# Kernel optimization log

Measured on AMD Instinct MI355X. Metric: run time of the kernel, lower is better.

The kernel has to match this reference:

```python
import jax, jax.numpy as jnp
import numpy as np

HEADS, DIM_HEAD = 8, 64  # per init_kwargs


def cdist(x, w):
    """Euclidean distance between rows of x [..., n, d] and w [m, d] -> [..., n, m].
    Matches torch.cdist (non-squared) / L2DistanceLinear(squared=False)."""
    sq = (x * x).sum(-1, keepdims=True) + (w * w).sum(-1) - 2.0 * (x @ w.T)
    return jnp.sqrt(jnp.maximum(sq, 0.0))


def setup_inputs() -> dict:
    key = jax.random.key(0)
    k1, k2, k3 = jax.random.split(key, 3)
    B, N, D = 4, 2048, 512
    dim_inner = HEADS * DIM_HEAD  # 512
    x = jax.random.normal(k1, (B, N, D), dtype=jnp.float32)
    w_qkv = jax.random.normal(k2, (3 * dim_inner, D), dtype=jnp.float32)
    w_out = jax.random.normal(k3, (D, dim_inner), dtype=jnp.float32)
    return {"x": x, "w_qkv": w_qkv, "w_out": w_out}


def reference(x, w_qkv, w_out):
    B, N, D = x.shape
    scale = DIM_HEAD ** -0.5

    # L2-distance QKV projection (cdist, non-squared, no negate/bias)
    qkv = cdist(x, w_qkv)                                  # [B, N, 3*H*DH]
    qkv = qkv.reshape(B, N, 3, HEADS, DIM_HEAD).transpose(2, 0, 3, 1, 4)  # [3, B, H, N, DH]
    q, k, v = qkv[0], qkv[1], qkv[2]

    # neg squared-L2 attention scores: -(||q||^2 + ||k||^2 - 2 q.k)
    q_sq = (q * q).sum(-1)                                 # [B, H, N]
    k_sq = (k * k).sum(-1)                                 # [B, H, N]
    dots = jnp.einsum('bhid,bhjd->bhij', q, k)             # [B, H, N, N]
    sim = -(q_sq[..., :, None] + k_sq[..., None, :] - 2.0 * dots) * scale

    attn = jax.nn.softmax(sim, axis=-1)
    out = jnp.einsum('bhij,bhjd->bhid', attn, v)           # [B, H, N, DH]
    out = out.transpose(0, 2, 1, 3).reshape(B, N, HEADS * DIM_HEAD)

    # L2-distance output projection
    return cdist(out, w_out)                               # [B, N, D]
```

## Files before the change

kernel.cpp:

```cpp
#include <hip/hip_runtime.h>
#include <stdint.h>

typedef float v4f  __attribute__((ext_vector_type(4)));
typedef float v16f __attribute__((ext_vector_type(16)));
typedef short v8s  __attribute__((ext_vector_type(8)));
typedef uint32_t u32;

#define DEVI static __device__ __forceinline__

DEVI unsigned short f2bf(float f) {
    u32 u = __builtin_bit_cast(u32, f);
    u = (u + 0x7fffu + ((u >> 16) & 1u)) >> 16;
    return (unsigned short)u;
}
DEVI float bf2f(unsigned short h) {
    u32 u = ((u32)h) << 16;
    return __builtin_bit_cast(float, u);
}

template <typename T>
DEVI void async16(const T* g, T* l) {
    __builtin_amdgcn_global_load_lds(
        (const __attribute__((address_space(1))) u32*)g,
        (__attribute__((address_space(3))) u32*)l, 16, 0, 0);
}

DEVI v4f bmfma(v8s a, v8s b, v4f c) {
    return __builtin_amdgcn_mfma_f32_16x16x32_bf16(a, b, c, 0, 0, 0);
}
DEVI v16f bmfma32(v8s a, v8s b, v16f c) {
    return __builtin_amdgcn_mfma_f32_32x32x16_bf16(a, b, c, 0, 0, 0);
}

#if __has_builtin(__builtin_amdgcn_permlane32_swap)
#define HAVE_PLSWAP 1
typedef unsigned int v2u __attribute__((ext_vector_type(2)));
#endif

DEVI void swap32(u32 a, u32 b, u32& lo, u32& hi) {
#ifdef HAVE_PLSWAP
    v2u r = __builtin_amdgcn_permlane32_swap(a, b, false, false);
    lo = r.x; hi = r.y;
#else
    u32 ax = __shfl_xor(a, 32), bx = __shfl_xor(b, 32);
    int hh = (threadIdx.x & 63) >> 5;
    lo = hh ? bx : a;
    hi = hh ? b : ax;
#endif
}

static const size_t HSZ = 32ull * 2048 * 64;

__launch_bounds__(256, 2)
__global__ void prep_all(const float* __restrict__ X, const float* __restrict__ WQ,
                         const float* __restrict__ WO,
                         unsigned short* __restrict__ Xb, unsigned short* __restrict__ WQb,
                         unsigned short* __restrict__ WOb,
                         float* __restrict__ xsq, float* __restrict__ wqsq,
                         float* __restrict__ wosq, float* __restrict__ wors)
{
    const int bid = blockIdx.x;
    const int w = threadIdx.x >> 6, lane = threadIdx.x & 63;
    const float* src; unsigned short* dst; float* Sq; float* Rs = nullptr;
    int r;
    if (bid < 2048)      { src = X;  dst = Xb;  Sq = xsq;  r = bid * 4 + w; }
    else if (bid < 2432) { src = WQ; dst = WQb; Sq = wqsq; r = (bid - 2048) * 4 + w; }
    else                 { src = WO; dst = WOb; Sq = wosq; Rs = wors; r = (bid - 2432) * 4 + w; }

    const float* xr = src + (size_t)r * 512 + lane * 8;
    float4 a = *(const float4*)xr;
    float4 c = *(const float4*)(xr + 4);
    float s = a.x*a.x + a.y*a.y + a.z*a.z + a.w*a.w
            + c.x*c.x + c.y*c.y + c.z*c.z + c.w*c.w;
    float sm = a.x + a.y + a.z + a.w + c.x + c.y + c.z + c.w;
    uint4 pkv;
    unsigned short* e = (unsigned short*)&pkv;
    e[0] = f2bf(a.x); e[1] = f2bf(a.y); e[2] = f2bf(a.z); e[3] = f2bf(a.w);
    e[4] = f2bf(c.x); e[5] = f2bf(c.y); e[6] = f2bf(c.z); e[7] = f2bf(c.w);
    *(uint4*)(dst + (size_t)r * 512 + lane * 8) = pkv;
#pragma unroll
    for (int d = 32; d > 0; d >>= 1) {
        s  += __shfl_xor(s, d);
        sm += __shfl_xor(sm, d);
    }
    if (lane == 0) { Sq[r] = s; if (Rs) Rs[r] = sm; }
}

__launch_bounds__(256, 2)
__global__ void gemm_cdist(const unsigned short* __restrict__ A,
                           const unsigned short* __restrict__ B,
                           const float* __restrict__ Asq,
                           const float* __restrict__ Bsq,
                           unsigned short* __restrict__ QKV,
                           float* __restrict__ Ksqc)
{
    __shared__ unsigned short lsm[2 * 2 * 128 * 32];
    const int t = threadIdx.x;
    const int lane = t & 63, w = t >> 6;
    const int low = lane & 15, quad = lane >> 4;
    const int wm = w & 1, wn = w >> 1;
    const int tM = blockIdx.x * 128, tN = blockIdx.y * 128;

    v4f acc[4][4];
#pragma unroll
    for (int a = 0; a < 4; ++a)
#pragma unroll
        for (int b = 0; b < 4; ++b) acc[a][b] = (v4f){0.f, 0.f, 0.f, 0.f};

    int kstage = 0;
    auto STAGE = [&](int buf) {
        unsigned short* lA = lsm + buf * 8192;
        unsigned short* lB = lA + 4096;
#pragma unroll
        for (int is = 0; is < 2; ++is) {
            int slot = is * 256 + t;
            int r = slot >> 2, bp = slot & 3, bs = bp ^ (r & 3);
            async16(A + (size_t)(tM + r) * 512 + kstage + bs * 8, lA + slot * 8);
            async16(B + (size_t)(tN + r) * 512 + kstage + bs * 8, lB + slot * 8);
        }
        kstage += 32;
    };

    STAGE(0);
    __syncthreads();

#pragma unroll 2
    for (int iter = 0; iter < 16; ++iter) {
        const int c = iter & 1;
        if (iter < 15) STAGE(1 - c);
        const unsigned short* lA = lsm + c * 8192;
        const unsigned short* lB = lA + 4096;

        v8s bfr[4];
#pragma unroll
        for (int ns = 0; ns < 4; ++ns) {
            int row = wn * 64 + ns * 16 + low;
            bfr[ns] = *(const v8s*)(lB + (row * 4 + (quad ^ (row & 3))) * 8);
        }
#pragma unroll
        for (int ms = 0; ms < 4; ++ms) {
            int row = wm * 64 + ms * 16 + low;
            v8s af = *(const v8s*)(lA + (row * 4 + (quad ^ (row & 3))) * 8);
#pragma unroll
            for (int ns = 0; ns < 4; ++ns)
                acc[ms][ns] = bmfma(af, bfr[ns], acc[ms][ns]);
        }
        __syncthreads();
    }

    const int tt = tN >> 9;
    if (tt != 2) {
#pragma unroll
        for (int ms = 0; ms < 4; ++ms) {
#pragma unroll
            for (int reg = 0; reg < 4; ++reg) {
                const int row = tM + wm * 64 + ms * 16 + quad * 4 + reg;
                const int b = row >> 11, i = row & 2047;
                float kacc = 0.f;
#pragma unroll
                for (int ns = 0; ns < 4; ++ns) {
                    const int col = tN + wn * 64 + ns * 16 + low;
                    float dot = acc[ms][ns][reg];
                    float val = sqrtf(fmaxf(Asq[row] + Bsq[col] - 2.f * dot, 0.f)) - 32.f;
                    int h = (col >> 6) & 7, d = col & 63, bh = b * 8 + h;
                    if (tt == 0) {
                        QKV[((size_t)bh * 2048 + i) * 64 + d] =
                            f2bf(val * 0.36067376022224085f);
                    } else {
                        QKV[HSZ + ((size_t)bh * 2048 + i) * 64 + d] = f2bf(val);
                        kacc += val * val;
                    }
                }
                if (tt == 1) {
#pragma unroll
                    for (int d = 1; d < 16; d <<= 1) kacc += __shfl_xor(kacc, d);
                    if (low == 0) {
                        int h = ((tN + wn * 64) >> 6) & 7;
                        Ksqc[(size_t)(b * 8 + h) * 2048 + i] = -kacc * 0.18033688011112042f;
                    }
                }
            }
        }
    } else {
        u32 packed[4][4][2];
#pragma unroll
        for (int ms = 0; ms < 4; ++ms)
#pragma unroll
            for (int ns = 0; ns < 4; ++ns) {
                const int col = tN + wn * 64 + ns * 16 + low;
                float bs_ = Bsq[col];
#pragma unroll
                for (int rp = 0; rp < 2; ++rp) {
                    u32 pk = 0;
#pragma unroll
                    for (int sub = 0; sub < 2; ++sub) {
                        int reg = rp * 2 + sub;
                        int row = tM + wm * 64 + ms * 16 + quad * 4 + reg;
                        float val = sqrtf(fmaxf(Asq[row] + bs_
                                                - 2.f * acc[ms][ns][reg], 0.f)) - 32.f;
                        pk |= (u32)f2bf(val) << (16 * sub);
                    }
                    packed[ms][ns][rp] = pk;
                }
            }
        u32* lT32 = (u32*)lsm;
#pragma unroll
        for (int p = 0; p < 2; ++p) {
            __syncthreads();
            if (wm == p) {
#pragma unroll
                for (int ms = 0; ms < 4; ++ms)
#pragma unroll
                    for (int ns = 0; ns < 4; ++ns) {
                        int cl = wn * 64 + ns * 16 + low;
#pragma unroll
                        for (int rp = 0; rp < 2; ++rp)
                            lT32[cl * 36 + ms * 8 + quad * 2 + rp] = packed[ms][ns][rp];
                    }
            }
            __syncthreads();
#pragma unroll
            for (int cc = 0; cc < 4; ++cc) {
                int col = cc * 32 + (t >> 3);
                int i0 = (t & 7) * 8;
                uint4 vvv = *(const uint4*)(lsm + col * 72 + i0);
                int colg = tN + col;
                int h = (colg >> 6) & 7, d = colg & 63;
                int rowg = tM + p * 64 + i0;
                int b = rowg >> 11, i = rowg & 2047;
                *(uint4*)(QKV + 2 * HSZ
                          + ((size_t)((b * 8 + h) * 64 + d)) * 2048 + i) = vvv;
            }
        }
    }
    (void)0;
}

__launch_bounds__(256, 2)
__global__ void flash_attn(const unsigned short* __restrict__ Q,
                           const unsigned short* __restrict__ K,
                           const unsigned short* __restrict__ VT,
                           const float* __restrict__ Ksqc,
                           unsigned short* __restrict__ OP,
                           float* __restrict__ Osqp)
{
    __shared__ unsigned short lK[2][64 * 64];
    __shared__ unsigned short lV[2][64 * 64];
    __shared__ float lKqA[2048];
    const int t = threadIdx.x, lane = t & 63, w = t >> 6;
    const int i31 = lane & 31, h = lane >> 5;
    const int qt = blockIdx.x, bh = blockIdx.y;
    const size_t base = (size_t)bh * (2048 * 64);
    const int row0 = qt * 128 + w * 32;

    v8s qfr[4];
#pragma unroll
    for (int kt = 0; kt < 4; ++kt)
        qfr[kt] = *(const v8s*)(Q + base + (size_t)(row0 + i31) * 64 + kt * 16 + h * 8);

    v16f o[2];
    float lacc = 0.f;
#pragma unroll
    for (int dt = 0; dt < 2; ++dt)
#pragma unroll
        for (int r = 0; r < 16; ++r) o[dt][r] = 0.f;

    const unsigned short* kg = K + base;
    const unsigned short* vg = VT + (size_t)bh * 64 * 2048;
    const float* kqg = Ksqc + (size_t)bh * 2048;

    auto STAGE = [&](int buf) {
#pragma unroll
        for (int is = 0; is < 2; ++is) {
            int slot = is * 256 + t;
            int r = slot >> 3, bp = slot & 7, bs = bp ^ (r & 7);
            async16(kg + (size_t)r * 64 + bs * 8, &lK[buf][slot * 8]);
        }
#pragma unroll
        for (int is = 0; is < 2; ++is) {
            int slot = is * 256 + t;
            int r = slot >> 3, bp = slot & 7, bs = bp ^ (r & 7);
            async16(vg + (size_t)r * 2048 + bs * 8, &lV[buf][slot * 8]);
        }
        kg += 64 * 64; vg += 64;
    };

#pragma unroll
    for (int is = 0; is < 2; ++is) {
        int slot = is * 256 + t;
        async16(kqg + slot * 4, lKqA + slot * 4);
    }
    STAGE(0);
    __syncthreads();

#pragma unroll 2
    for (int iter = 0; iter < 32; ++iter) {
        const int c = iter & 1;

        asm volatile("s_waitcnt lgkmcnt(0)" ::: "memory");
        __builtin_amdgcn_s_barrier();
        if (iter < 31) {
            STAGE(1 - c);
            asm volatile("s_waitcnt vmcnt(4)" ::: "memory");
        } else {
            asm volatile("s_waitcnt vmcnt(0)" ::: "memory");
        }
        __builtin_amdgcn_s_barrier();
        __builtin_amdgcn_sched_barrier(0);

#pragma unroll
        for (int T = 0; T < 2; ++T) {
            const int jrow = T * 32 + i31;
            v8s kf[4];
#pragma unroll
            for (int kt = 0; kt < 4; ++kt)
                kf[kt] = *(const v8s*)(&lK[c][(jrow * 8 + ((2 * kt + h) ^ (jrow & 7))) * 8]);

            v16f sa;
#pragma unroll
            for (int r1 = 0; r1 < 4; ++r1) {
                v4f kq = *(const v4f*)(&lKqA[iter * 64 + T * 32 + r1 * 8 + h * 4]);
#pragma unroll
                for (int u = 0; u < 4; ++u) sa[4 * r1 + u] = kq[u];
            }
#pragma unroll
            for (int kt = 0; kt < 4; ++kt)
                sa = bmfma32(kf[kt], qfr[kt], sa);
            u32 pk[8];
#pragma unroll
            for (int r1 = 0; r1 < 4; ++r1) {
                float p0 = exp2f(sa[4 * r1 + 0]);
                float p1 = exp2f(sa[4 * r1 + 1]);
                float p2 = exp2f(sa[4 * r1 + 2]);
                float p3 = exp2f(sa[4 * r1 + 3]);
                lacc += (p0 + p1) + (p2 + p3);
                pk[2 * r1] = __builtin_amdgcn_perm(
                    __builtin_bit_cast(u32, p1), __builtin_bit_cast(u32, p0),
                    0x07060302u);
                pk[2 * r1 + 1] = __builtin_amdgcn_perm(
                    __builtin_bit_cast(u32, p3), __builtin_bit_cast(u32, p2),
                    0x07060302u);
            }
#pragma unroll
            for (int c2 = 0; c2 < 2; ++c2) {
                const int jb = 2 * (2 * T + c2);
                v8s vf[2];
#pragma unroll
                for (int dt = 0; dt < 2; ++dt) {
                    const int drow = dt * 32 + i31;
                    vf[dt] = *(const v8s*)(&lV[c][(drow * 8 + ((jb + h) ^ (drow & 7))) * 8]);
                }
                uint4 dd;
                swap32(pk[4 * c2 + 0], pk[4 * c2 + 2], dd.x, dd.z);
                swap32(pk[4 * c2 + 1], pk[4 * c2 + 3], dd.y, dd.w);
                v8s af = __builtin_bit_cast(v8s, dd);
                o[0] = bmfma32(af, vf[0], o[0]);
                o[1] = bmfma32(af, vf[1], o[1]);
            }
        }
    }

    const int b = bh >> 3, hh = bh & 7;
    lacc += __shfl_xor(lacc, 32);
    unsigned short* ob = OP + ((size_t)(b * 2048 + row0)) * 512 + hh * 64;
    float* osq = Osqp + (size_t)hh * 8192 + b * 2048 + row0;
#pragma unroll
    for (int r = 0; r < 16; ++r) {
        const int rl = (r & 3) + 8 * (r >> 2) + 4 * h;
        float inv = 1.f / __shfl(lacc, rl);
        unsigned short e0 = f2bf(o[0][r] * inv);
        unsigned short e1 = f2bf(o[1][r] * inv);
        ob[(size_t)rl * 512 + i31] = e0;
        ob[(size_t)rl * 512 + 32 + i31] = e1;
        float f0 = bf2f(e0) + 32.f, f1 = bf2f(e1) + 32.f;
        float s = f0 * f0 + f1 * f1;
        s += __shfl_xor(s, 1);  s += __shfl_xor(s, 2);  s += __shfl_xor(s, 4);
        s += __shfl_xor(s, 8);  s += __shfl_xor(s, 16);
        if (i31 == 0) osq[rl] = s;
    }
}

__launch_bounds__(256, 2)
__global__ void gemm_out(const unsigned short* __restrict__ A,
                         const unsigned short* __restrict__ B,
                         const float* __restrict__ Osqp,
                         const float* __restrict__ Bsq,
                         const float* __restrict__ Brs,
                         float* __restrict__ OUT)
{
    __shared__ unsigned short lA[2][128 * 64];
    __shared__ unsigned short lB[2][64 * 64];
    __shared__ float lAsq[128];
    const int t = threadIdx.x;
    const int lane = t & 63, w = t >> 6;
    const int low = lane & 15, quad = lane >> 4;
    const int wm = w & 1, wn = w >> 1;
    const int tM = blockIdx.x * 128, tN = blockIdx.y * 64;

    if (t < 128) {
        float s = 0.f;
#pragma unroll
        for (int hh = 0; hh < 8; ++hh) s += Osqp[(size_t)hh * 8192 + tM + t];
        lAsq[t] = s;
    }

    v4f acc[4][2];
#pragma unroll
    for (int a = 0; a < 4; ++a)
#pragma unroll
        for (int b = 0; b < 2; ++b) acc[a][b] = (v4f){0.f, 0.f, 0.f, 0.f};

    int kstage = 0;
    auto STAGE = [&](int buf) {
#pragma unroll
        for (int is = 0; is < 4; ++is) {
            int slot = is * 256 + t;
            int r = slot >> 3, bp = slot & 7, bs = bp ^ (r & 7);
            async16(A + (size_t)(tM + r) * 512 + kstage + bs * 8, &lA[buf][slot * 8]);
        }
#pragma unroll
        for (int is = 0; is < 2; ++is) {
            int slot = is * 256 + t;
            int r = slot >> 3, bp = slot & 7, bs = bp ^ (r & 7);
            async16(B + (size_t)(tN + r) * 512 + kstage + bs * 8, &lB[buf][slot * 8]);
        }
        kstage += 64;
    };

    STAGE(0);
    __syncthreads();

#pragma unroll 2
    for (int iter = 0; iter < 8; ++iter) {
        const int c = iter & 1;
        if (iter < 7) STAGE(1 - c);

        v8s bfr[2][2];
#pragma unroll
        for (int ns = 0; ns < 2; ++ns) {
            int row = wn * 32 + ns * 16 + low;
#pragma unroll
            for (int kc = 0; kc < 2; ++kc)
                bfr[ns][kc] = *(const v8s*)(&lB[c][(row * 8 + ((kc * 4 + quad) ^ (row & 7))) * 8]);
        }
#pragma unroll
        for (int ms = 0; ms < 4; ++ms) {
            int row = wm * 64 + ms * 16 + low;
            v8s af0 = *(const v8s*)(&lA[c][(row * 8 + ((0 + quad) ^ (row & 7))) * 8]);
            v8s af1 = *(const v8s*)(&lA[c][(row * 8 + ((4 + quad) ^ (row & 7))) * 8]);
#pragma unroll
            for (int ns = 0; ns < 2; ++ns) {
                acc[ms][ns] = bmfma(af0, bfr[ns][0], acc[ms][ns]);
                acc[ms][ns] = bmfma(af1, bfr[ns][1], acc[ms][ns]);
            }
        }
        __syncthreads();
    }

#pragma unroll
    for (int ms = 0; ms < 4; ++ms) {
#pragma unroll
        for (int ns = 0; ns < 2; ++ns) {
#pragma unroll
            for (int reg = 0; reg < 4; ++reg) {
                int rloc = wm * 64 + ms * 16 + quad * 4 + reg;
                int row = tM + rloc;
                int col = tN + wn * 32 + ns * 16 + low;
                float val = sqrtf(fmaxf(lAsq[rloc] + Bsq[col]
                                        - 2.f * (acc[ms][ns][reg] + 32.f * Brs[col]), 0.f));
                OUT[(size_t)row * 512 + col] = val;
            }
        }
    }
}

extern "C" void kernel_launch(void* const* d_in, const int* in_sizes, int n_in,
                              void* d_out, int out_size, void* d_ws, size_t ws_size,
                              hipStream_t stream)
{
    const float* x    = (const float*)d_in[0];
    const float* wqkv = (const float*)d_in[1];
    const float* wout = (const float*)d_in[2];
    float* out = (float*)d_out;

    char* ws = (char*)d_ws;
    size_t off = 0;
    auto alloc = [&](size_t bytes) -> void* {
        void* p = ws + off;
        off += (bytes + 255) & ~(size_t)255;
        return p;
    };
    unsigned short* xb   = (unsigned short*)alloc(8192ull * 512 * 2);
    unsigned short* wqb  = (unsigned short*)alloc(1536ull * 512 * 2);
    unsigned short* wob  = (unsigned short*)alloc(512ull * 512 * 2);
    unsigned short* qkv  = (unsigned short*)alloc(3ull * HSZ * 2);
    unsigned short* outp = (unsigned short*)alloc(8192ull * 512 * 2);
    float* xsq  = (float*)alloc(8192 * 4);
    float* wqsq = (float*)alloc(1536 * 4);
    float* wosq = (float*)alloc(512 * 4);
    float* wors = (float*)alloc(512 * 4);
    float* ksqc = (float*)alloc(65536ull * 4);
    float* osqp = (float*)alloc(8ull * 8192 * 4);

    prep_all<<<2560, 256, 0, stream>>>(x, wqkv, wout, xb, wqb, wob,
                                       xsq, wqsq, wosq, wors);

    gemm_cdist<<<dim3(64, 12), 256, 0, stream>>>(xb, wqb, xsq, wqsq, qkv, ksqc);
    flash_attn<<<dim3(16, 32), 256, 0, stream>>>(qkv, qkv + HSZ, qkv + 2 * HSZ,
                                                 ksqc, outp, osqp);
    gemm_out<<<dim3(64, 8), 256, 0, stream>>>(outp, wob, osqp, wosq, wors, out);
}
```

Measured before the change: 170.7 us.

## Interleave two QK score tiles in flash attention and remap block IDs for locality

The inner loop now issues both 32-row QK^T MFMA chains up front, so the second tile's score matmul can overlap with the exp/PV work of the first instead of running strictly in sequence. The launch moves to a 1D grid with a remapped block index that spreads heads across XCDs and keeps same-head query tiles together, aiming for better K/V cache reuse. The cost is higher register pressure from holding two score accumulators and two sets of K fragments, which could hurt occupancy under the 256x2 launch bounds.

```diff
diff --git a/kernel.cpp b/kernel.cpp
--- a/kernel.cpp
+++ b/kernel.cpp
@@ -249,7 +249,9 @@
     __shared__ float lKqA[2048];
     const int t = threadIdx.x, lane = t & 63, w = t >> 6;
     const int i31 = lane & 31, h = lane >> 5;
-    const int qt = blockIdx.x, bh = blockIdx.y;
+    const int bid = blockIdx.x;
+    const int bh = (bid & 7) * 4 + (bid >> 7);
+    const int qt = (bid >> 3) & 15;
     const size_t base = (size_t)bh * (2048 * 64);
     const int row0 = qt * 128 + w * 32;
 
@@ -308,55 +310,91 @@
         __builtin_amdgcn_s_barrier();
         __builtin_amdgcn_sched_barrier(0);
 
-#pragma unroll
-        for (int T = 0; T < 2; ++T) {
-            const int jrow = T * 32 + i31;
-            v8s kf[4];
-#pragma unroll
-            for (int kt = 0; kt < 4; ++kt)
-                kf[kt] = *(const v8s*)(&lK[c][(jrow * 8 + ((2 * kt + h) ^ (jrow & 7))) * 8]);
-
-            v16f sa;
-#pragma unroll
-            for (int r1 = 0; r1 < 4; ++r1) {
-                v4f kq = *(const v4f*)(&lKqA[iter * 64 + T * 32 + r1 * 8 + h * 4]);
-#pragma unroll
-                for (int u = 0; u < 4; ++u) sa[4 * r1 + u] = kq[u];
-            }
-#pragma unroll
-            for (int kt = 0; kt < 4; ++kt)
-                sa = bmfma32(kf[kt], qfr[kt], sa);
-            u32 pk[8];
-#pragma unroll
-            for (int r1 = 0; r1 < 4; ++r1) {
-                float p0 = exp2f(sa[4 * r1 + 0]);
-                float p1 = exp2f(sa[4 * r1 + 1]);
-                float p2 = exp2f(sa[4 * r1 + 2]);
-                float p3 = exp2f(sa[4 * r1 + 3]);
-                lacc += (p0 + p1) + (p2 + p3);
-                pk[2 * r1] = __builtin_amdgcn_perm(
-                    __builtin_bit_cast(u32, p1), __builtin_bit_cast(u32, p0),
-                    0x07060302u);
-                pk[2 * r1 + 1] = __builtin_amdgcn_perm(
-                    __builtin_bit_cast(u32, p3), __builtin_bit_cast(u32, p2),
-                    0x07060302u);
-            }
-#pragma unroll
-            for (int c2 = 0; c2 < 2; ++c2) {
-                const int jb = 2 * (2 * T + c2);
-                v8s vf[2];
-#pragma unroll
-                for (int dt = 0; dt < 2; ++dt) {
-                    const int drow = dt * 32 + i31;
-                    vf[dt] = *(const v8s*)(&lV[c][(drow * 8 + ((jb + h) ^ (drow & 7))) * 8]);
-                }
-                uint4 dd;
-                swap32(pk[4 * c2 + 0], pk[4 * c2 + 2], dd.x, dd.z);
-                swap32(pk[4 * c2 + 1], pk[4 * c2 + 3], dd.y, dd.w);
-                v8s af = __builtin_bit_cast(v8s, dd);
-                o[0] = bmfma32(af, vf[0], o[0]);
-                o[1] = bmfma32(af, vf[1], o[1]);
-            }
+        const int jrow0 = i31, jrow1 = 32 + i31;
+        v8s kf0[4], kf1[4];
+#pragma unroll
+        for (int kt = 0; kt < 4; ++kt) {
+            kf0[kt] = *(const v8s*)(&lK[c][(jrow0 * 8 + ((2 * kt + h) ^ (jrow0 & 7))) * 8]);
+            kf1[kt] = *(const v8s*)(&lK[c][(jrow1 * 8 + ((2 * kt + h) ^ (jrow1 & 7))) * 8]);
+        }
+        v16f sa0, sa1;
+#pragma unroll
+        for (int r1 = 0; r1 < 4; ++r1) {
+            v4f kq0 = *(const v4f*)(&lKqA[iter * 64 + r1 * 8 + h * 4]);
+            v4f kq1 = *(const v4f*)(&lKqA[iter * 64 + 32 + r1 * 8 + h * 4]);
+#pragma unroll
+            for (int u = 0; u < 4; ++u) {
+                sa0[4 * r1 + u] = kq0[u];
+                sa1[4 * r1 + u] = kq1[u];
+            }
+        }
+#pragma unroll
+        for (int kt = 0; kt < 4; ++kt) sa0 = bmfma32(kf0[kt], qfr[kt], sa0);
+#pragma unroll
+        for (int kt = 0; kt < 4; ++kt) sa1 = bmfma32(kf1[kt], qfr[kt], sa1);
+
+        u32 pk0[8];
+#pragma unroll
+        for (int r1 = 0; r1 < 4; ++r1) {
+            float p0 = exp2f(sa0[4 * r1 + 0]);
+            float p1 = exp2f(sa0[4 * r1 + 1]);
+            float p2 = exp2f(sa0[4 * r1 + 2]);
+            float p3 = exp2f(sa0[4 * r1 + 3]);
+            lacc += (p0 + p1) + (p2 + p3);
+            pk0[2 * r1] = __builtin_amdgcn_perm(
+                __builtin_bit_cast(u32, p1), __builtin_bit_cast(u32, p0),
+                0x07060302u);
+            pk0[2 * r1 + 1] = __builtin_amdgcn_perm(
+                __builtin_bit_cast(u32, p3), __builtin_bit_cast(u32, p2),
+                0x07060302u);
+        }
+#pragma unroll
+        for (int c2 = 0; c2 < 2; ++c2) {
+            const int jb = 2 * c2;
+            v8s vf[2];
+#pragma unroll
+            for (int dt = 0; dt < 2; ++dt) {
+                const int drow = dt * 32 + i31;
+                vf[dt] = *(const v8s*)(&lV[c][(drow * 8 + ((jb + h) ^ (drow & 7))) * 8]);
+            }
+            uint4 dd;
+            swap32(pk0[4 * c2 + 0], pk0[4 * c2 + 2], dd.x, dd.z);
+            swap32(pk0[4 * c2 + 1], pk0[4 * c2 + 3], dd.y, dd.w);
+            v8s af = __builtin_bit_cast(v8s, dd);
+            o[0] = bmfma32(af, vf[0], o[0]);
+            o[1] = bmfma32(af, vf[1], o[1]);
+        }
+
+        u32 pk1[8];
+#pragma unroll
+        for (int r1 = 0; r1 < 4; ++r1) {
+            float p0 = exp2f(sa1[4 * r1 + 0]);
+            float p1 = exp2f(sa1[4 * r1 + 1]);
+            float p2 = exp2f(sa1[4 * r1 + 2]);
+            float p3 = exp2f(sa1[4 * r1 + 3]);
+            lacc += (p0 + p1) + (p2 + p3);
+            pk1[2 * r1] = __builtin_amdgcn_perm(
+                __builtin_bit_cast(u32, p1), __builtin_bit_cast(u32, p0),
+                0x07060302u);
+            pk1[2 * r1 + 1] = __builtin_amdgcn_perm(
+                __builtin_bit_cast(u32, p3), __builtin_bit_cast(u32, p2),
+                0x07060302u);
+        }
+#pragma unroll
+        for (int c2 = 0; c2 < 2; ++c2) {
+            const int jb = 4 + 2 * c2;
+            v8s vf[2];
+#pragma unroll
+            for (int dt = 0; dt < 2; ++dt) {
+                const int drow = dt * 32 + i31;
+                vf[dt] = *(const v8s*)(&lV[c][(drow * 8 + ((jb + h) ^ (drow & 7))) * 8]);
+            }
+            uint4 dd;
+            swap32(pk1[4 * c2 + 0], pk1[4 * c2 + 2], dd.x, dd.z);
+            swap32(pk1[4 * c2 + 1], pk1[4 * c2 + 3], dd.y, dd.w);
+            v8s af = __builtin_bit_cast(v8s, dd);
+            o[0] = bmfma32(af, vf[0], o[0]);
+            o[1] = bmfma32(af, vf[1], o[1]);
         }
     }
 
@@ -506,7 +544,7 @@
                                        xsq, wqsq, wosq, wors);
 
     gemm_cdist<<<dim3(64, 12), 256, 0, stream>>>(xb, wqb, xsq, wqsq, qkv, ksqc);
-    flash_attn<<<dim3(16, 32), 256, 0, stream>>>(qkv, qkv + HSZ, qkv + 2 * HSZ,
-                                                 ksqc, outp, osqp);
+    flash_attn<<<512, 256, 0, stream>>>(qkv, qkv + HSZ, qkv + 2 * HSZ,
+                                        ksqc, outp, osqp);
     gemm_out<<<dim3(64, 8), 256, 0, stream>>>(outp, wob, osqp, wosq, wors, out);
 }
```

After: 169.6 us. No clear change (-0.6%).
